# Optimization experiments

Hardware: AMD Instinct MI355X
Metric: run time of the kernel (lower is better)

Reference implementation:

```python
import jax, jax.numpy as jnp
import numpy as np

H = 16          # N_heads (Attention default)
DH = 32         # d per head (Attention default)
EPS = 1e-5      # torch LayerNorm eps
SCALE = float(1.0 / np.sqrt(DH))


def _ln(z, w, b):
    # LayerNorm over the last TWO dims (normalized_shape=(N_x, channel)), affine w/b of shape [2S, C]
    m = jnp.mean(z, axis=(-2, -1), keepdims=True)
    v = jnp.mean(jnp.square(z - m), axis=(-2, -1), keepdims=True)
    return (z - m) * jax.lax.rsqrt(v + EPS) * w + b


def _attention(a, p):
    # a: [2S, C]. Faithful to source: y = x.clone(), scores are NOT softmaxed (causal_mask=False).
    lx_w, lx_b, ly_w, ly_b, lf_w, lf_b, wq_w, wq_b, wk_w, wk_b, wv_w, wv_b, w1, b1, w2, b2, w3, b3 = p
    L = a.shape[0]
    xn = _ln(a, lx_w, lx_b)
    yn = _ln(a, ly_w, ly_b)
    q = (xn @ wq_w.T + wq_b).reshape(L, H, DH).transpose(1, 0, 2)  # [H, 2S, d]
    k = (yn @ wk_w.T + wk_b).reshape(L, H, DH).transpose(1, 0, 2)
    v = (yn @ wv_w.T + wv_b).reshape(L, H, DH).transpose(1, 0, 2)
    scores = jnp.einsum('hqd,hkd->hqk', q, k) * SCALE               # no softmax in source
    o = jnp.einsum('hqk,hkd->hqd', scores, v).transpose(1, 0, 2).reshape(L, H * DH)
    x1 = a + o @ w1.T + b1
    h = jax.nn.gelu(_ln(x1, lf_w, lf_b) @ w2.T + b2, approximate=False)
    return x1 + h @ w3.T + b3


def _forward(x, params):
    # x: [3, S, S, C]; params are stacked over the idx axis [S, ...] (one Attention per idx, shared across modes)
    S = x.shape[1]
    attn = jax.vmap(_attention, in_axes=(0, 0))
    for m1, m2 in [(0, 1), (2, 0), (1, 2)]:
        a = jnp.concatenate([x[m1], jnp.swapaxes(x[m2], 0, 1)], axis=1)  # [S, 2S, C]
        c = attn(a, params)                                              # [S, 2S, C]
        x = x.at[m1].set(c[:, :S, :])
        x = x.at[m2].set(c[:, S:, :])
    return x


def setup_inputs() -> dict:
    S, C, W = 16, 1024, 4
    D = H * DH   # 512
    L = 2 * S    # 32
    key = jax.random.key(0)
    ks = jax.random.split(key, 8)
    rn = lambda k, shp, s: jax.random.normal(k, shp, dtype=jnp.float32) * s
    return {
        'x': rn(ks[0], (3, S, S, C), 1.0),
        'lx_w': jnp.ones((S, L, C), jnp.float32), 'lx_b': jnp.zeros((S, L, C), jnp.float32),
        'ly_w': jnp.ones((S, L, C), jnp.float32), 'ly_b': jnp.zeros((S, L, C), jnp.float32),
        'lf_w': jnp.ones((S, L, C), jnp.float32), 'lf_b': jnp.zeros((S, L, C), jnp.float32),
        'wq_w': rn(ks[1], (S, D, C), 0.02), 'wq_b': jnp.zeros((S, D), jnp.float32),
        'wk_w': rn(ks[2], (S, D, C), 0.02), 'wk_b': jnp.zeros((S, D), jnp.float32),
        'wv_w': rn(ks[3], (S, D, C), 0.02), 'wv_b': jnp.zeros((S, D), jnp.float32),
        'w1': rn(ks[4], (S, C, D), 0.02), 'b1': jnp.zeros((S, C), jnp.float32),
        'w2': rn(ks[5], (S, W * C, C), 0.02), 'b2': jnp.zeros((S, W * C), jnp.float32),
        'w3': rn(ks[6], (S, C, W * C), 0.02), 'b3': jnp.zeros((S, C), jnp.float32),
    }


def reference(x, lx_w, lx_b, ly_w, ly_b, lf_w, lf_b, wq_w, wq_b, wk_w, wk_b, wv_w, wv_b, w1, b1, w2, b2, w3, b3):
    params = (lx_w, lx_b, ly_w, ly_b, lf_w, lf_b, wq_w, wq_b, wk_w, wk_b, wv_w, wv_b, w1, b1, w2, b2, w3, b3)
    return _forward(x, params)
```

## Files before the change

kernel.cpp:

```cpp
#include <hip/hip_runtime.h>


#define C1024 1024
#define D512  512
#define FF4096 4096
#define NELEM 32768.0f
#define EPSLN 1e-5f
#define QSCALE 0.17677669529663687f
#define LP 258

typedef __attribute__((ext_vector_type(8))) short bf16x8;
typedef __attribute__((ext_vector_type(4))) float f32x4;
typedef unsigned short u16;

__device__ inline u16 f2bf(float f) {
    unsigned u = __float_as_uint(f);
    u += 0x7fffu + ((u >> 16) & 1u);
    return (u16)(u >> 16);
}

__device__ inline bf16x8 cvt8(f32x4 a, f32x4 b) {
    bf16x8 r;
    r[0] = (short)f2bf(a[0]); r[1] = (short)f2bf(a[1]);
    r[2] = (short)f2bf(a[2]); r[3] = (short)f2bf(a[3]);
    r[4] = (short)f2bf(b[0]); r[5] = (short)f2bf(b[1]);
    r[6] = (short)f2bf(b[2]); r[7] = (short)f2bf(b[3]);
    return r;
}

struct Cvt4 {
    const float* s[4];
    u16* d[4];
    int N32[4], kzs[4], base[4];
};
__global__ void __launch_bounds__(256, 8) k_cvt6(Cvt4 a) {
    __shared__ float lds[16 * LP];
    int bid = blockIdx.x;
    int ts = 0;
#pragma unroll
    for (int j = 1; j < 4; ++j) if (bid >= a.base[j]) ts = j;
    int local = bid - a.base[ts];
    int kzs = a.kzs[ts], N32 = a.N32[ts];
    int kz = local % kzs;
    int b  = (local / kzs) & 1;
    int nt = (local / (kzs * 2)) % N32;
    int i  = local / (kzs * 2 * N32);
    int K = kzs * 256;
    int t = threadIdx.x;
    int row = t >> 4, c16 = t & 15;
    const float* Sp = a.s[ts] + ((size_t)((i * N32 + nt) * 32) + b * 16 + row) * K + kz * 256 + c16 * 4;
    float* Lrow = lds + row * LP + c16 * 4;
#pragma unroll
    for (int j = 0; j < 4; ++j) {
        f32x4 v = *(const f32x4*)(Sp + 64 * j);
        Lrow[64 * j]     = v[0];
        Lrow[64 * j + 1] = v[1];
        Lrow[64 * j + 2] = v[2];
        Lrow[64 * j + 3] = v[3];
    }
    __syncthreads();
    u16* Dp = a.d[ts] + (((size_t)(i * N32 + nt) * (kzs * 8) + kz * 8) * 1024) + b * 512;
#pragma unroll
    for (int p = 0; p < 2; ++p) {
        int u = p * 2048 + t * 8;
        int c   = u >> 9;
        int rem = u & 511;
        int kg = rem >> 7;
        int lr = (rem >> 3) & 15;
        const float* src = lds + lr * LP + c * 32 + kg * 8;
        f32x4 lo, hi;
        lo[0] = src[0]; lo[1] = src[1]; lo[2] = src[2]; lo[3] = src[3];
        hi[0] = src[4]; hi[1] = src[5]; hi[2] = src[6]; hi[3] = src[7];
        *(bf16x8*)(Dp + c * 1024 + rem) = cvt8(lo, hi);
    }
}

template<int EPI>
__global__ void __launch_bounds__(256, 4)
k_cvtgemm(const float* __restrict__ W32, u16* __restrict__ W16,
          const u16* __restrict__ act, int kzs, int N32,
          const float* __restrict__ bias,
          u16* __restrict__ hb,
          const float* __restrict__ x1, float* __restrict__ xout,
          int m1, int m2) {
    __shared__ float lds[16 * LP];
    __shared__ float Pl[4][32][16];
    int bx = blockIdx.x, i = blockIdx.y;
    int b = bx & 1, nt = bx >> 1;
    int K = kzs * 256;
    int t = threadIdx.x;
    int w = t >> 6, lane = t & 63;
    int lr = lane & 15, kg = lane >> 4;
    int row = t >> 4, c16 = t & 15;
    const float* Sp = W32 + ((size_t)(i * N32 + nt) * 32 + b * 16 + row) * K + c16 * 4;
    u16* Dbase = W16 + ((size_t)(i * N32 + nt) * (kzs * 8)) * 1024 + b * 512;
    const u16* A0 = act + ((size_t)(i * 32) + lr) * K + kg * 8;
    const u16* A1 = A0 + (size_t)16 * K;
    f32x4 acc0 = {0.f, 0.f, 0.f, 0.f}, acc1 = {0.f, 0.f, 0.f, 0.f};
    float* Lrow = lds + row * LP + c16 * 4;
    const float* src = lds + lr * LP + kg * 8;
    for (int kz = 0; kz < kzs; ++kz) {
        const float* Sk = Sp + kz * 256;
#pragma unroll
        for (int j = 0; j < 4; ++j) {
            f32x4 v = *(const f32x4*)(Sk + 64 * j);
            Lrow[64 * j]     = v[0];
            Lrow[64 * j + 1] = v[1];
            Lrow[64 * j + 2] = v[2];
            Lrow[64 * j + 3] = v[3];
        }
        __syncthreads();
        u16* Dp = Dbase + (size_t)(kz * 8) * 1024;
#pragma unroll
        for (int p = 0; p < 2; ++p) {
            int c = p * 4 + w;
            const float* s8 = src + c * 32;
            f32x4 lo, hi;
            lo[0] = s8[0]; lo[1] = s8[1]; lo[2] = s8[2]; lo[3] = s8[3];
            hi[0] = s8[4]; hi[1] = s8[5]; hi[2] = s8[6]; hi[3] = s8[7];
            bf16x8 r = cvt8(lo, hi);
            *(bf16x8*)(Dp + c * 1024 + lane * 8) = r;
            int kk = kz * 8 + c;
            bf16x8 aF0 = *(const bf16x8*)(A0 + kk * 32);
            bf16x8 aF1 = *(const bf16x8*)(A1 + kk * 32);
            acc0 = __builtin_amdgcn_mfma_f32_16x16x32_bf16(aF0, r, acc0, 0, 0, 0);
            acc1 = __builtin_amdgcn_mfma_f32_16x16x32_bf16(aF1, r, acc1, 0, 0, 0);
        }
        __syncthreads();
    }
#pragma unroll
    for (int rr = 0; rr < 4; ++rr) {
        Pl[w][kg * 4 + rr][lr]      = acc0[rr];
        Pl[w][16 + kg * 4 + rr][lr] = acc1[rr];
    }
    __syncthreads();
    int m = t >> 3, nl0 = (t & 7) * 2;
#pragma unroll
    for (int jj = 0; jj < 2; ++jj) {
        int nl = nl0 + jj;
        float v = Pl[0][m][nl] + Pl[1][m][nl] + Pl[2][m][nl] + Pl[3][m][nl];
        int n = nt * 32 + b * 16 + nl;
        if constexpr (EPI == 0) {
            float tt = v + bias[i * FF4096 + n];
            float g = 0.5f * tt * (1.f + erff(tt * 0.70710678118654752f));
            hb[((size_t)(i * 32) + m) * FF4096 + n] = f2bf(g);
        } else {
            int base = ((i * 32 + m) << 10) + n;
            float vv = v + bias[i * C1024 + n] + x1[base];
            int dst = (m < 16) ? (((m1 * 16 + i) * 16 + m) << 10)
                               : (((m2 * 16 + i) * 16 + (m - 16)) << 10);
            xout[dst + n] = vv;
        }
    }
}

__device__ inline void mmz(const u16* __restrict__ act, const u16* __restrict__ p,
                           int nkk, f32x4& acc0, f32x4& acc1) {
#pragma unroll 4
    for (int j = 0; j < nkk; ++j) {
        bf16x8 aF = *(const bf16x8*)(act + j * 32);
        bf16x8 b0 = *(const bf16x8*)(p + (size_t)j * 1024);
        bf16x8 b1 = *(const bf16x8*)(p + (size_t)j * 1024 + 512);
        acc0 = __builtin_amdgcn_mfma_f32_16x16x32_bf16(aF, b0, acc0, 0, 0, 0);
        acc1 = __builtin_amdgcn_mfma_f32_16x16x32_bf16(aF, b1, acc1, 0, 0, 0);
    }
}

__device__ inline void reduce256(float& s, float& q, int t, float* lds) {
    for (int off = 32; off; off >>= 1) {
        s += __shfl_down(s, off, 64);
        q += __shfl_down(q, off, 64);
    }
    int wv = t >> 6;
    if ((t & 63) == 0) { lds[wv * 2] = s; lds[wv * 2 + 1] = q; }
    __syncthreads();
    if (t == 0) {
        lds[8] = lds[0] + lds[2] + lds[4] + lds[6];
        lds[9] = lds[1] + lds[3] + lds[5] + lds[7];
    }
    __syncthreads();
    s = lds[8]; q = lds[9];
}

__global__ void k_ln1(const float* __restrict__ s1, const float* __restrict__ s2,
                      const float* __restrict__ gw, const float* __restrict__ gb,
                      const float* __restrict__ hw, const float* __restrict__ hb,
                      float* __restrict__ a_buf,
                      u16* __restrict__ xn, u16* __restrict__ yn) {
    __shared__ float lds[10];
    int i = blockIdx.x, cb = blockIdx.y, t = threadIdx.x;
    float s = 0.f, q = 0.f;
#pragma unroll 4
    for (int rr = 0; rr < 32; ++rr) {
        const float* src = (rr < 16)
            ? (s1 + ((i * 16 + rr) << 10))
            : (s2 + (((rr - 16) * 16 + i) << 10));
        f32x4 v = *(const f32x4*)(src + t * 4);
        s += v[0] + v[1] + v[2] + v[3];
        q += v[0]*v[0] + v[1]*v[1] + v[2]*v[2] + v[3]*v[3];
        if ((t >> 5) == cb)
            *(f32x4*)(a_buf + ((i * 32 + rr) << 10) + t * 4) = v;
    }
    reduce256(s, q, t, lds);
    float mean = s * (1.f / NELEM);
    float var = q * (1.f / NELEM) - mean * mean;
    float inv = rsqrtf(var + EPSLN);
    int c = cb * 128 + (t & 31) * 4;
    int r0 = (t >> 5) * 4;
#pragma unroll
    for (int rr = 0; rr < 4; ++rr) {
        int row = r0 + rr;
        const float* src = (row < 16)
            ? (s1 + ((i * 16 + row) << 10))
            : (s2 + (((row - 16) * 16 + i) << 10));
        f32x4 v = *(const f32x4*)(src + c);
        int base = ((i * 32 + row) << 10) + c;
        f32x4 gwv = *(const f32x4*)(gw + base);
        f32x4 gbv = *(const f32x4*)(gb + base);
        f32x4 hwv = *(const f32x4*)(hw + base);
        f32x4 hbv = *(const f32x4*)(hb + base);
        float z0 = (v[0]-mean)*inv, z1 = (v[1]-mean)*inv, z2 = (v[2]-mean)*inv, z3 = (v[3]-mean)*inv;
        uint2 a, b;
        a.x = (unsigned)f2bf(z0*gwv[0]+gbv[0]) | ((unsigned)f2bf(z1*gwv[1]+gbv[1]) << 16);
        a.y = (unsigned)f2bf(z2*gwv[2]+gbv[2]) | ((unsigned)f2bf(z3*gwv[3]+gbv[3]) << 16);
        b.x = (unsigned)f2bf(z0*hwv[0]+hbv[0]) | ((unsigned)f2bf(z1*hwv[1]+hbv[1]) << 16);
        b.y = (unsigned)f2bf(z2*hwv[2]+hbv[2]) | ((unsigned)f2bf(z3*hwv[3]+hbv[3]) << 16);
        *(uint2*)(xn + base) = a;
        *(uint2*)(yn + base) = b;
    }
}

__global__ void k_ln2(const float* __restrict__ x1,
                      const float* __restrict__ gw, const float* __restrict__ gb,
                      u16* __restrict__ out) {
    __shared__ float lds[10];
    int i = blockIdx.x, cb = blockIdx.y, t = threadIdx.x;
    float s = 0.f, q = 0.f;
#pragma unroll 4
    for (int rr = 0; rr < 32; ++rr) {
        f32x4 v = *(const f32x4*)(x1 + ((i * 32 + rr) << 10) + t * 4);
        s += v[0] + v[1] + v[2] + v[3];
        q += v[0]*v[0] + v[1]*v[1] + v[2]*v[2] + v[3]*v[3];
    }
    reduce256(s, q, t, lds);
    float mean = s * (1.f / NELEM);
    float var = q * (1.f / NELEM) - mean * mean;
    float inv = rsqrtf(var + EPSLN);
    int c = cb * 128 + (t & 31) * 4;
    int r0 = (t >> 5) * 4;
#pragma unroll
    for (int rr = 0; rr < 4; ++rr) {
        int base = ((i * 32 + r0 + rr) << 10) + c;
        f32x4 v  = *(const f32x4*)(x1 + base);
        f32x4 gwv = *(const f32x4*)(gw + base);
        f32x4 gbv = *(const f32x4*)(gb + base);
        float z0 = (v[0]-mean)*inv, z1 = (v[1]-mean)*inv, z2 = (v[2]-mean)*inv, z3 = (v[3]-mean)*inv;
        uint2 a;
        a.x = (unsigned)f2bf(z0*gwv[0]+gbv[0]) | ((unsigned)f2bf(z1*gwv[1]+gbv[1]) << 16);
        a.y = (unsigned)f2bf(z2*gwv[2]+gbv[2]) | ((unsigned)f2bf(z3*gwv[3]+gbv[3]) << 16);
        *(uint2*)(out + base) = a;
    }
}

__global__ void __launch_bounds__(512, 4)
k_gemm_qkv(const u16* __restrict__ xn, const u16* __restrict__ yn,
           const u16* __restrict__ wq, const float* __restrict__ wqb,
           const u16* __restrict__ wk, const float* __restrict__ wkb,
           const u16* __restrict__ wv, const float* __restrict__ wvb,
           u16* __restrict__ qo, u16* __restrict__ ko, u16* __restrict__ vT) {
    __shared__ float Pl[2][32][64];
    int bx = blockIdx.x, i = blockIdx.y;
    int w = threadIdx.x >> 6, lane = threadIdx.x & 63;
    int kh = w >> 2, mh = (w >> 1) & 1, wn = w & 1;
    int lr = lane & 15, kg = lane >> 4;
    int sel = bx >> 3;
    int ntl = (bx - sel * 8) * 2 + wn;
    const u16* act = (sel == 0 ? xn : yn) + (i * 32 + mh * 16 + lr) * C1024 + kh * 512 + kg * 8;
    const u16* Wm = (sel == 0 ? wq : (sel == 1 ? wk : wv));
    const u16* p = Wm + (((size_t)i * 16 + ntl) * 32 + kh * 16) * 1024 + lane * 8;
    f32x4 a0 = {0.f, 0.f, 0.f, 0.f}, a1 = {0.f, 0.f, 0.f, 0.f};
    mmz(act, p, 16, a0, a1);
    int m0 = mh * 16 + kg * 4;
#pragma unroll
    for (int r = 0; r < 4; ++r) {
        Pl[kh][m0 + r][wn * 32 + lr] = a0[r];
        Pl[kh][m0 + r][wn * 32 + 16 + lr] = a1[r];
    }
    __syncthreads();
    int t = threadIdx.x;
    int row = t >> 4, c0 = (t & 15) * 4;
    int nloc = bx * 64 - sel * 512 + c0;
    const float* bias = (sel == 0 ? wqb : (sel == 1 ? wkb : wvb)) + i * D512 + nloc;
    float v0 = Pl[0][row][c0]     + Pl[1][row][c0]     + bias[0];
    float v1 = Pl[0][row][c0 + 1] + Pl[1][row][c0 + 1] + bias[1];
    float v2 = Pl[0][row][c0 + 2] + Pl[1][row][c0 + 2] + bias[2];
    float v3 = Pl[0][row][c0 + 3] + Pl[1][row][c0 + 3] + bias[3];
    if (sel == 0) {
        uint2 a;
        a.x = (unsigned)f2bf(v0 * QSCALE) | ((unsigned)f2bf(v1 * QSCALE) << 16);
        a.y = (unsigned)f2bf(v2 * QSCALE) | ((unsigned)f2bf(v3 * QSCALE) << 16);
        *(uint2*)(qo + (i * 32 + row) * D512 + nloc) = a;
    } else if (sel == 1) {
        uint2 a;
        a.x = (unsigned)f2bf(v0) | ((unsigned)f2bf(v1) << 16);
        a.y = (unsigned)f2bf(v2) | ((unsigned)f2bf(v3) << 16);
        *(uint2*)(ko + (i * 32 + row) * D512 + nloc) = a;
    } else {
        int h = nloc >> 5, d = nloc & 31;
        u16* vb = vT + ((i * 16 + h) * 32 + d) * 32 + row;
        vb[0]  = f2bf(v0);
        vb[32] = f2bf(v1);
        vb[64] = f2bf(v2);
        vb[96] = f2bf(v3);
    }
}

__global__ void k_attn(const u16* __restrict__ q, const u16* __restrict__ k,
                       const u16* __restrict__ vT, u16* __restrict__ o) {
    __shared__ __align__(16) u16 Sm[4][32][32];
    int i = blockIdx.x;
    int w = threadIdx.x >> 6, lane = threadIdx.x & 63;
    int h = blockIdx.y * 4 + w;
    int lr = lane & 15, kg = lane >> 4;
    const u16* qb = q + i * 32 * D512 + h * 32 + kg * 8;
    const u16* kb = k + i * 32 * D512 + h * 32 + kg * 8;
    bf16x8 a0 = *(const bf16x8*)(qb + lr * D512);
    bf16x8 a1 = *(const bf16x8*)(qb + (16 + lr) * D512);
    bf16x8 b0 = *(const bf16x8*)(kb + lr * D512);
    bf16x8 b1 = *(const bf16x8*)(kb + (16 + lr) * D512);
    f32x4 z = {0.f, 0.f, 0.f, 0.f};
    f32x4 s00 = __builtin_amdgcn_mfma_f32_16x16x32_bf16(a0, b0, z, 0, 0, 0);
    f32x4 s01 = __builtin_amdgcn_mfma_f32_16x16x32_bf16(a0, b1, z, 0, 0, 0);
    f32x4 s10 = __builtin_amdgcn_mfma_f32_16x16x32_bf16(a1, b0, z, 0, 0, 0);
    f32x4 s11 = __builtin_amdgcn_mfma_f32_16x16x32_bf16(a1, b1, z, 0, 0, 0);
    int mr = kg * 4;
#pragma unroll
    for (int r = 0; r < 4; ++r) {
        Sm[w][mr + r][lr]           = f2bf(s00[r]);
        Sm[w][mr + r][16 + lr]      = f2bf(s01[r]);
        Sm[w][16 + mr + r][lr]      = f2bf(s10[r]);
        Sm[w][16 + mr + r][16 + lr] = f2bf(s11[r]);
    }
    __syncthreads();
    bf16x8 p0 = *(const bf16x8*)&Sm[w][lr][kg * 8];
    bf16x8 p1 = *(const bf16x8*)&Sm[w][16 + lr][kg * 8];
    const u16* vb = vT + (i * 16 + h) * 32 * 32 + kg * 8;
    bf16x8 v0 = *(const bf16x8*)(vb + lr * 32);
    bf16x8 v1 = *(const bf16x8*)(vb + (16 + lr) * 32);
    f32x4 o00 = __builtin_amdgcn_mfma_f32_16x16x32_bf16(p0, v0, z, 0, 0, 0);
    f32x4 o01 = __builtin_amdgcn_mfma_f32_16x16x32_bf16(p0, v1, z, 0, 0, 0);
    f32x4 o10 = __builtin_amdgcn_mfma_f32_16x16x32_bf16(p1, v0, z, 0, 0, 0);
    f32x4 o11 = __builtin_amdgcn_mfma_f32_16x16x32_bf16(p1, v1, z, 0, 0, 0);
#pragma unroll
    for (int r = 0; r < 4; ++r) {
        o[(i * 32 + mr + r) * D512 + h * 32 + lr]           = f2bf(o00[r]);
        o[(i * 32 + mr + r) * D512 + h * 32 + 16 + lr]      = f2bf(o01[r]);
        o[(i * 32 + 16 + mr + r) * D512 + h * 32 + lr]      = f2bf(o10[r]);
        o[(i * 32 + 16 + mr + r) * D512 + h * 32 + 16 + lr] = f2bf(o11[r]);
    }
}

__global__ void __launch_bounds__(512, 4)
k_gemm_w1(const u16* __restrict__ ob, const u16* __restrict__ W,
          const float* __restrict__ bias, const float* __restrict__ a_buf,
          float* __restrict__ x1) {
    __shared__ float Pl[2][32][64];
    int bx = blockIdx.x, i = blockIdx.y;
    int w = threadIdx.x >> 6, lane = threadIdx.x & 63;
    int kh = w >> 2, mh = (w >> 1) & 1, wn = w & 1;
    int lr = lane & 15, kg = lane >> 4;
    int nt = bx * 2 + wn;
    const u16* act = ob + (i * 32 + mh * 16 + lr) * D512 + kh * 256 + kg * 8;
    const u16* p = W + (((size_t)i * 32 + nt) * 16 + kh * 8) * 1024 + lane * 8;
    f32x4 a0 = {0.f, 0.f, 0.f, 0.f}, a1 = {0.f, 0.f, 0.f, 0.f};
    mmz(act, p, 8, a0, a1);
    int m0 = mh * 16 + kg * 4;
#pragma unroll
    for (int r = 0; r < 4; ++r) {
        Pl[kh][m0 + r][wn * 32 + lr] = a0[r];
        Pl[kh][m0 + r][wn * 32 + 16 + lr] = a1[r];
    }
    __syncthreads();
    int t = threadIdx.x;
    int row = t >> 4, c0 = (t & 15) * 4;
    int n = bx * 64 + c0;
    int base = ((i * 32 + row) << 10) + n;
    f32x4 bv = *(const f32x4*)(bias + i * C1024 + n);
    f32x4 av = *(const f32x4*)(a_buf + base);
    f32x4 r;
    r[0] = Pl[0][row][c0]     + Pl[1][row][c0]     + bv[0] + av[0];
    r[1] = Pl[0][row][c0 + 1] + Pl[1][row][c0 + 1] + bv[1] + av[1];
    r[2] = Pl[0][row][c0 + 2] + Pl[1][row][c0 + 2] + bv[2] + av[2];
    r[3] = Pl[0][row][c0 + 3] + Pl[1][row][c0 + 3] + bv[3] + av[3];
    *(f32x4*)(x1 + base) = r;
}

__global__ void __launch_bounds__(256, 4)
k_gemm_w2(const u16* __restrict__ lnf, const u16* __restrict__ W,
          const float* __restrict__ bias, u16* __restrict__ hb) {
    int bx = blockIdx.x, i = blockIdx.y;
    int w = threadIdx.x >> 6, lane = threadIdx.x & 63;
    int mh = w & 1, wn = w >> 1, lr = lane & 15, kg = lane >> 4;
    int nt = bx * 2 + wn;
    const u16* act = lnf + (i * 32 + mh * 16 + lr) * C1024 + kg * 8;
    const u16* p = W + (((size_t)i * 128 + nt) * 32) * 1024 + lane * 8;
    f32x4 a0 = {0.f, 0.f, 0.f, 0.f}, a1 = {0.f, 0.f, 0.f, 0.f};
    mmz(act, p, 32, a0, a1);
    int m0 = mh * 16 + kg * 4;
    int nb = bx * 64 + wn * 32;
    int n0 = nb + lr, n1 = nb + 16 + lr;
    float b0 = bias[i * FF4096 + n0], b1 = bias[i * FF4096 + n1];
#pragma unroll
    for (int r = 0; r < 4; ++r) {
        float t0 = a0[r] + b0;
        float t1 = a1[r] + b1;
        float g0 = 0.5f * t0 * (1.f + erff(t0 * 0.70710678118654752f));
        float g1 = 0.5f * t1 * (1.f + erff(t1 * 0.70710678118654752f));
        hb[(i * 32 + m0 + r) * FF4096 + n0] = f2bf(g0);
        hb[(i * 32 + m0 + r) * FF4096 + n1] = f2bf(g1);
    }
}

__global__ void __launch_bounds__(1024, 4)
k_gemm_w3(const u16* __restrict__ hb, const u16* __restrict__ W,
          const float* __restrict__ bias, const float* __restrict__ x1,
          float* __restrict__ xout, int m1, int m2) {
    __shared__ float Pl[4][32][64];
    int bx = blockIdx.x, i = blockIdx.y;
    int w = threadIdx.x >> 6, lane = threadIdx.x & 63;
    int kq = w >> 2, mh = (w >> 1) & 1, wn = w & 1;
    int lr = lane & 15, kg = lane >> 4;
    int nt = bx * 2 + wn;
    const u16* act = hb + (i * 32 + mh * 16 + lr) * FF4096 + kq * 1024 + kg * 8;
    const u16* p = W + (((size_t)i * 32 + nt) * 128 + kq * 32) * 1024 + lane * 8;
    f32x4 a0 = {0.f, 0.f, 0.f, 0.f}, a1 = {0.f, 0.f, 0.f, 0.f};
    mmz(act, p, 32, a0, a1);
    int m0 = mh * 16 + kg * 4;
#pragma unroll
    for (int r = 0; r < 4; ++r) {
        Pl[kq][m0 + r][wn * 32 + lr] = a0[r];
        Pl[kq][m0 + r][wn * 32 + 16 + lr] = a1[r];
    }
    __syncthreads();
    int t = threadIdx.x;
    int row = t >> 5, c0 = (t & 31) * 2;
    int n = bx * 64 + c0;
    int dst = (row < 16) ? (((m1 * 16 + i) * 16 + row) << 10)
                         : (((m2 * 16 + i) * 16 + (row - 16)) << 10);
    int base = ((i * 32 + row) << 10) + n;
#pragma unroll
    for (int j = 0; j < 2; ++j) {
        float v = Pl[0][row][c0 + j] + Pl[1][row][c0 + j]
                + Pl[2][row][c0 + j] + Pl[3][row][c0 + j]
                + bias[i * C1024 + n + j] + x1[base + j];
        xout[dst + n + j] = v;
    }
}

extern "C" void kernel_launch(void* const* d_in, const int* in_sizes, int n_in,
                              void* d_out, int out_size, void* d_ws, size_t ws_size,
                              hipStream_t stream) {
    const float* x_in = (const float*)d_in[0];
    const float* lx_w = (const float*)d_in[1];
    const float* lx_b = (const float*)d_in[2];
    const float* ly_w = (const float*)d_in[3];
    const float* ly_b = (const float*)d_in[4];
    const float* lf_w = (const float*)d_in[5];
    const float* lf_b = (const float*)d_in[6];
    const float* wq_w = (const float*)d_in[7];
    const float* wq_b = (const float*)d_in[8];
    const float* wk_w = (const float*)d_in[9];
    const float* wk_b = (const float*)d_in[10];
    const float* wv_w = (const float*)d_in[11];
    const float* wv_b = (const float*)d_in[12];
    const float* w1   = (const float*)d_in[13];
    const float* b1   = (const float*)d_in[14];
    const float* w2   = (const float*)d_in[15];
    const float* b2   = (const float*)d_in[16];
    const float* w3   = (const float*)d_in[17];
    const float* b3   = (const float*)d_in[18];

    float* xbuf = (float*)d_out;
    char* ws = (char*)d_ws;
    float* a_buf  = (float*)(ws);
    float* x1_buf = (float*)(ws + (2u << 20));
    u16*   xn     = (u16*)(ws + (4u << 20));
    u16*   yn     = (u16*)(ws + (5u << 20));
    u16*   lnf    = (u16*)(ws + (6u << 20));
    u16*   qb     = (u16*)(ws + (7u << 20));
    u16*   kb     = (u16*)(ws + 7 * (1u << 20) + (1u << 19));
    u16*   vT     = (u16*)(ws + (8u << 20));
    u16*   ob     = (u16*)(ws + 8 * (1u << 20) + (1u << 19));
    u16*   hbuf   = (u16*)(ws + (9u << 20));
    u16*   wq16   = (u16*)(ws + (16u  << 20));
    u16*   wk16   = (u16*)(ws + (32u  << 20));
    u16*   wv16   = (u16*)(ws + (48u  << 20));
    u16*   w1_16  = (u16*)(ws + (64u  << 20));
    u16*   w2_16  = (u16*)(ws + (80u  << 20));
    u16*   w3_16  = (u16*)(ws + (208u << 20));

    Cvt4 ca;
    ca.s[0] = wq_w; ca.d[0] = wq16;  ca.N32[0] = 16;  ca.kzs[0] = 4;  ca.base[0] = 0;
    ca.s[1] = wk_w; ca.d[1] = wk16;  ca.N32[1] = 16;  ca.kzs[1] = 4;  ca.base[1] = 2048;
    ca.s[2] = wv_w; ca.d[2] = wv16;  ca.N32[2] = 16;  ca.kzs[2] = 4;  ca.base[2] = 4096;
    ca.s[3] = w1;   ca.d[3] = w1_16; ca.N32[3] = 32;  ca.kzs[3] = 2;  ca.base[3] = 6144;
    k_cvt6<<<8192, 256, 0, stream>>>(ca);

    const size_t SLAB = (size_t)16 * 16 * 1024;
    const int modes[3][2] = {{0, 1}, {2, 0}, {1, 2}};
    for (int mi = 0; mi < 3; ++mi) {
        int m1 = modes[mi][0], m2 = modes[mi][1];
        const float* s1 = (mi == 2) ? (xbuf + m1 * SLAB) : (x_in + m1 * SLAB);
        const float* s2 = (mi == 0) ? (x_in + m2 * SLAB) : (xbuf + m2 * SLAB);
        k_ln1<<<dim3(16, 8), 256, 0, stream>>>(s1, s2, lx_w, lx_b, ly_w, ly_b, a_buf, xn, yn);
        k_gemm_qkv<<<dim3(24, 16), 512, 0, stream>>>(xn, yn, wq16, wq_b, wk16, wk_b, wv16, wv_b, qb, kb, vT);
        k_attn<<<dim3(16, 4), 256, 0, stream>>>(qb, kb, vT, ob);
        k_gemm_w1<<<dim3(16, 16), 512, 0, stream>>>(ob, w1_16, b1, a_buf, x1_buf);
        k_ln2<<<dim3(16, 8), 256, 0, stream>>>(x1_buf, lf_w, lf_b, lnf);
        if (mi == 0) {
            k_cvtgemm<0><<<dim3(256, 16), 256, 0, stream>>>(
                w2, w2_16, lnf, 4, 128, b2, hbuf, nullptr, nullptr, 0, 0);
            k_cvtgemm<1><<<dim3(64, 16), 256, 0, stream>>>(
                w3, w3_16, hbuf, 16, 32, b3, nullptr, x1_buf, xbuf, m1, m2);
        } else {
            k_gemm_w2<<<dim3(64, 16), 256, 0, stream>>>(lnf, w2_16, b2, hbuf);
            k_gemm_w3<<<dim3(16, 16), 1024, 0, stream>>>(hbuf, w3_16, b3, x1_buf, xbuf, m1, m2);
        }
    }
}
```

Baseline: 507.5 us.

## Fuse QKV and W1 weight conversion into first-pass GEMMs, prefetch weights

Removes the standalone fp32-to-bf16 conversion kernel for Wq/Wk/Wv/W1. Each weight is now converted inside the first mode's GEMM, which writes the bf16 copy while using it, the same way W2/W3 were already handled. This saves one full pass over those weights and one launch. The shared conversion-GEMM body also register-prefetches the next K-chunk of fp32 weights before the LDS conversion, so global loads overlap the MFMA work. In exchange, the first-mode QKV and W1 GEMMs use a slower narrow-tile path.

```diff
diff --git a/kernel.cpp b/kernel.cpp
--- a/kernel.cpp
+++ b/kernel.cpp
@@ -28,88 +28,33 @@
     return r;
 }
 
-struct Cvt4 {
-    const float* s[4];
-    u16* d[4];
-    int N32[4], kzs[4], base[4];
-};
-__global__ void __launch_bounds__(256, 8) k_cvt6(Cvt4 a) {
-    __shared__ float lds[16 * LP];
-    int bid = blockIdx.x;
-    int ts = 0;
-#pragma unroll
-    for (int j = 1; j < 4; ++j) if (bid >= a.base[j]) ts = j;
-    int local = bid - a.base[ts];
-    int kzs = a.kzs[ts], N32 = a.N32[ts];
-    int kz = local % kzs;
-    int b  = (local / kzs) & 1;
-    int nt = (local / (kzs * 2)) % N32;
-    int i  = local / (kzs * 2 * N32);
-    int K = kzs * 256;
-    int t = threadIdx.x;
+__device__ inline void cvtgemm_body(const float* __restrict__ Sp,
+                                    u16* __restrict__ Dbase,
+                                    const u16* __restrict__ A0,
+                                    const u16* __restrict__ A1,
+                                    int kzs, int t, int w, int lane,
+                                    float* lds, f32x4& acc0, f32x4& acc1) {
     int row = t >> 4, c16 = t & 15;
-    const float* Sp = a.s[ts] + ((size_t)((i * N32 + nt) * 32) + b * 16 + row) * K + kz * 256 + c16 * 4;
-    float* Lrow = lds + row * LP + c16 * 4;
-#pragma unroll
-    for (int j = 0; j < 4; ++j) {
-        f32x4 v = *(const f32x4*)(Sp + 64 * j);
-        Lrow[64 * j]     = v[0];
-        Lrow[64 * j + 1] = v[1];
-        Lrow[64 * j + 2] = v[2];
-        Lrow[64 * j + 3] = v[3];
-    }
-    __syncthreads();
-    u16* Dp = a.d[ts] + (((size_t)(i * N32 + nt) * (kzs * 8) + kz * 8) * 1024) + b * 512;
-#pragma unroll
-    for (int p = 0; p < 2; ++p) {
-        int u = p * 2048 + t * 8;
-        int c   = u >> 9;
-        int rem = u & 511;
-        int kg = rem >> 7;
-        int lr = (rem >> 3) & 15;
-        const float* src = lds + lr * LP + c * 32 + kg * 8;
-        f32x4 lo, hi;
-        lo[0] = src[0]; lo[1] = src[1]; lo[2] = src[2]; lo[3] = src[3];
-        hi[0] = src[4]; hi[1] = src[5]; hi[2] = src[6]; hi[3] = src[7];
-        *(bf16x8*)(Dp + c * 1024 + rem) = cvt8(lo, hi);
-    }
-}
-
-template<int EPI>
-__global__ void __launch_bounds__(256, 4)
-k_cvtgemm(const float* __restrict__ W32, u16* __restrict__ W16,
-          const u16* __restrict__ act, int kzs, int N32,
-          const float* __restrict__ bias,
-          u16* __restrict__ hb,
-          const float* __restrict__ x1, float* __restrict__ xout,
-          int m1, int m2) {
-    __shared__ float lds[16 * LP];
-    __shared__ float Pl[4][32][16];
-    int bx = blockIdx.x, i = blockIdx.y;
-    int b = bx & 1, nt = bx >> 1;
-    int K = kzs * 256;
-    int t = threadIdx.x;
-    int w = t >> 6, lane = t & 63;
-    int lr = lane & 15, kg = lane >> 4;
-    int row = t >> 4, c16 = t & 15;
-    const float* Sp = W32 + ((size_t)(i * N32 + nt) * 32 + b * 16 + row) * K + c16 * 4;
-    u16* Dbase = W16 + ((size_t)(i * N32 + nt) * (kzs * 8)) * 1024 + b * 512;
-    const u16* A0 = act + ((size_t)(i * 32) + lr) * K + kg * 8;
-    const u16* A1 = A0 + (size_t)16 * K;
-    f32x4 acc0 = {0.f, 0.f, 0.f, 0.f}, acc1 = {0.f, 0.f, 0.f, 0.f};
+    int lr = lane & 15, kg = lane >> 4;
     float* Lrow = lds + row * LP + c16 * 4;
     const float* src = lds + lr * LP + kg * 8;
+    f32x4 rv0 = *(const f32x4*)(Sp);
+    f32x4 rv1 = *(const f32x4*)(Sp + 64);
+    f32x4 rv2 = *(const f32x4*)(Sp + 128);
+    f32x4 rv3 = *(const f32x4*)(Sp + 192);
     for (int kz = 0; kz < kzs; ++kz) {
-        const float* Sk = Sp + kz * 256;
-#pragma unroll
-        for (int j = 0; j < 4; ++j) {
-            f32x4 v = *(const f32x4*)(Sk + 64 * j);
-            Lrow[64 * j]     = v[0];
-            Lrow[64 * j + 1] = v[1];
-            Lrow[64 * j + 2] = v[2];
-            Lrow[64 * j + 3] = v[3];
+        Lrow[0]   = rv0[0]; Lrow[1]   = rv0[1]; Lrow[2]   = rv0[2]; Lrow[3]   = rv0[3];
+        Lrow[64]  = rv1[0]; Lrow[65]  = rv1[1]; Lrow[66]  = rv1[2]; Lrow[67]  = rv1[3];
+        Lrow[128] = rv2[0]; Lrow[129] = rv2[1]; Lrow[130] = rv2[2]; Lrow[131] = rv2[3];
+        Lrow[192] = rv3[0]; Lrow[193] = rv3[1]; Lrow[194] = rv3[2]; Lrow[195] = rv3[3];
+        __syncthreads();
+        if (kz + 1 < kzs) {
+            const float* Sk = Sp + (kz + 1) * 256;
+            rv0 = *(const f32x4*)(Sk);
+            rv1 = *(const f32x4*)(Sk + 64);
+            rv2 = *(const f32x4*)(Sk + 128);
+            rv3 = *(const f32x4*)(Sk + 192);
         }
-        __syncthreads();
         u16* Dp = Dbase + (size_t)(kz * 8) * 1024;
 #pragma unroll
         for (int p = 0; p < 2; ++p) {
@@ -128,6 +73,31 @@
         }
         __syncthreads();
     }
+}
+
+template<int EPI>
+__global__ void __launch_bounds__(256, 4)
+k_cvtgemm(const float* __restrict__ W32, u16* __restrict__ W16,
+          const u16* __restrict__ act, int kzs, int N32,
+          const float* __restrict__ bias,
+          u16* __restrict__ hb,
+          const float* __restrict__ x1, float* __restrict__ xout,
+          const float* __restrict__ a_buf,
+          int m1, int m2) {
+    __shared__ float lds[16 * LP];
+    __shared__ float Pl[4][32][16];
+    int bx = blockIdx.x, i = blockIdx.y;
+    int b = bx & 1, nt = bx >> 1;
+    int K = kzs * 256;
+    int t = threadIdx.x;
+    int w = t >> 6, lane = t & 63;
+    int lr = lane & 15, kg = lane >> 4;
+    const float* Sp = W32 + ((size_t)(i * N32 + nt) * 32 + b * 16 + (t >> 4)) * K + (t & 15) * 4;
+    u16* Dbase = W16 + ((size_t)(i * N32 + nt) * (kzs * 8)) * 1024 + b * 512;
+    const u16* A0 = act + ((size_t)(i * 32) + lr) * K + kg * 8;
+    const u16* A1 = A0 + (size_t)16 * K;
+    f32x4 acc0 = {0.f, 0.f, 0.f, 0.f}, acc1 = {0.f, 0.f, 0.f, 0.f};
+    cvtgemm_body(Sp, Dbase, A0, A1, kzs, t, w, lane, lds, acc0, acc1);
 #pragma unroll
     for (int rr = 0; rr < 4; ++rr) {
         Pl[w][kg * 4 + rr][lr]      = acc0[rr];
@@ -144,12 +114,67 @@
             float tt = v + bias[i * FF4096 + n];
             float g = 0.5f * tt * (1.f + erff(tt * 0.70710678118654752f));
             hb[((size_t)(i * 32) + m) * FF4096 + n] = f2bf(g);
-        } else {
+        } else if constexpr (EPI == 1) {
             int base = ((i * 32 + m) << 10) + n;
             float vv = v + bias[i * C1024 + n] + x1[base];
             int dst = (m < 16) ? (((m1 * 16 + i) * 16 + m) << 10)
                                : (((m2 * 16 + i) * 16 + (m - 16)) << 10);
             xout[dst + n] = vv;
+        } else {
+            int base = ((i * 32 + m) << 10) + n;
+            xout[base] = v + bias[i * C1024 + n] + a_buf[base];
+        }
+    }
+}
+
+__global__ void __launch_bounds__(256, 4)
+k_cvtgemm_qkv(const float* __restrict__ wq32, const float* __restrict__ wk32,
+              const float* __restrict__ wv32,
+              u16* __restrict__ wq16, u16* __restrict__ wk16, u16* __restrict__ wv16,
+              const u16* __restrict__ xn, const u16* __restrict__ yn,
+              const float* __restrict__ wqb, const float* __restrict__ wkb,
+              const float* __restrict__ wvb,
+              u16* __restrict__ qo, u16* __restrict__ ko, u16* __restrict__ vT) {
+    __shared__ float lds[16 * LP];
+    __shared__ float Pl[4][32][16];
+    const int kzs = 4, N32 = 16, K = 1024;
+    int bx = blockIdx.x, i = blockIdx.y;
+    int sel = bx >> 5;
+    int bxl = bx & 31;
+    int b = bxl & 1, nt = bxl >> 1;
+    const float* W32 = (sel == 0 ? wq32 : (sel == 1 ? wk32 : wv32));
+    u16* W16 = (sel == 0 ? wq16 : (sel == 1 ? wk16 : wv16));
+    const u16* act = (sel == 0 ? xn : yn);
+    const float* bias = (sel == 0 ? wqb : (sel == 1 ? wkb : wvb));
+    int t = threadIdx.x;
+    int w = t >> 6, lane = t & 63;
+    int lr = lane & 15, kg = lane >> 4;
+    const float* Sp = W32 + ((size_t)(i * N32 + nt) * 32 + b * 16 + (t >> 4)) * K + (t & 15) * 4;
+    u16* Dbase = W16 + ((size_t)(i * N32 + nt) * (kzs * 8)) * 1024 + b * 512;
+    const u16* A0 = act + ((size_t)(i * 32) + lr) * K + kg * 8;
+    const u16* A1 = A0 + (size_t)16 * K;
+    f32x4 acc0 = {0.f, 0.f, 0.f, 0.f}, acc1 = {0.f, 0.f, 0.f, 0.f};
+    cvtgemm_body(Sp, Dbase, A0, A1, kzs, t, w, lane, lds, acc0, acc1);
+#pragma unroll
+    for (int rr = 0; rr < 4; ++rr) {
+        Pl[w][kg * 4 + rr][lr]      = acc0[rr];
+        Pl[w][16 + kg * 4 + rr][lr] = acc1[rr];
+    }
+    __syncthreads();
+    int m = t >> 3, nl0 = (t & 7) * 2;
+#pragma unroll
+    for (int jj = 0; jj < 2; ++jj) {
+        int nl = nl0 + jj;
+        float v = Pl[0][m][nl] + Pl[1][m][nl] + Pl[2][m][nl] + Pl[3][m][nl];
+        int n = nt * 32 + b * 16 + nl;
+        v += bias[i * D512 + n];
+        if (sel == 0) {
+            qo[(i * 32 + m) * D512 + n] = f2bf(v * QSCALE);
+        } else if (sel == 1) {
+            ko[(i * 32 + m) * D512 + n] = f2bf(v);
+        } else {
+            int h = n >> 5, d = n & 31;
+            vT[((i * 16 + h) * 32 + d) * 32 + m] = f2bf(v);
         }
     }
 }
@@ -499,13 +524,6 @@
     u16*   w2_16  = (u16*)(ws + (80u  << 20));
     u16*   w3_16  = (u16*)(ws + (208u << 20));
 
-    Cvt4 ca;
-    ca.s[0] = wq_w; ca.d[0] = wq16;  ca.N32[0] = 16;  ca.kzs[0] = 4;  ca.base[0] = 0;
-    ca.s[1] = wk_w; ca.d[1] = wk16;  ca.N32[1] = 16;  ca.kzs[1] = 4;  ca.base[1] = 2048;
-    ca.s[2] = wv_w; ca.d[2] = wv16;  ca.N32[2] = 16;  ca.kzs[2] = 4;  ca.base[2] = 4096;
-    ca.s[3] = w1;   ca.d[3] = w1_16; ca.N32[3] = 32;  ca.kzs[3] = 2;  ca.base[3] = 6144;
-    k_cvt6<<<8192, 256, 0, stream>>>(ca);
-
     const size_t SLAB = (size_t)16 * 16 * 1024;
     const int modes[3][2] = {{0, 1}, {2, 0}, {1, 2}};
     for (int mi = 0; mi < 3; ++mi) {
@@ -513,16 +531,23 @@
         const float* s1 = (mi == 2) ? (xbuf + m1 * SLAB) : (x_in + m1 * SLAB);
         const float* s2 = (mi == 0) ? (x_in + m2 * SLAB) : (xbuf + m2 * SLAB);
         k_ln1<<<dim3(16, 8), 256, 0, stream>>>(s1, s2, lx_w, lx_b, ly_w, ly_b, a_buf, xn, yn);
-        k_gemm_qkv<<<dim3(24, 16), 512, 0, stream>>>(xn, yn, wq16, wq_b, wk16, wk_b, wv16, wv_b, qb, kb, vT);
-        k_attn<<<dim3(16, 4), 256, 0, stream>>>(qb, kb, vT, ob);
-        k_gemm_w1<<<dim3(16, 16), 512, 0, stream>>>(ob, w1_16, b1, a_buf, x1_buf);
-        k_ln2<<<dim3(16, 8), 256, 0, stream>>>(x1_buf, lf_w, lf_b, lnf);
         if (mi == 0) {
+            k_cvtgemm_qkv<<<dim3(96, 16), 256, 0, stream>>>(
+                wq_w, wk_w, wv_w, wq16, wk16, wv16, xn, yn,
+                wq_b, wk_b, wv_b, qb, kb, vT);
+            k_attn<<<dim3(16, 4), 256, 0, stream>>>(qb, kb, vT, ob);
+            k_cvtgemm<2><<<dim3(64, 16), 256, 0, stream>>>(
+                w1, w1_16, ob, 2, 32, b1, nullptr, nullptr, x1_buf, a_buf, 0, 0);
+            k_ln2<<<dim3(16, 8), 256, 0, stream>>>(x1_buf, lf_w, lf_b, lnf);
             k_cvtgemm<0><<<dim3(256, 16), 256, 0, stream>>>(
-                w2, w2_16, lnf, 4, 128, b2, hbuf, nullptr, nullptr, 0, 0);
+                w2, w2_16, lnf, 4, 128, b2, hbuf, nullptr, nullptr, nullptr, 0, 0);
             k_cvtgemm<1><<<dim3(64, 16), 256, 0, stream>>>(
-                w3, w3_16, hbuf, 16, 32, b3, nullptr, x1_buf, xbuf, m1, m2);
+                w3, w3_16, hbuf, 16, 32, b3, nullptr, x1_buf, xbuf, nullptr, m1, m2);
         } else {
+            k_gemm_qkv<<<dim3(24, 16), 512, 0, stream>>>(xn, yn, wq16, wq_b, wk16, wk_b, wv16, wv_b, qb, kb, vT);
+            k_attn<<<dim3(16, 4), 256, 0, stream>>>(qb, kb, vT, ob);
+            k_gemm_w1<<<dim3(16, 16), 512, 0, stream>>>(ob, w1_16, b1, a_buf, x1_buf);
+            k_ln2<<<dim3(16, 8), 256, 0, stream>>>(x1_buf, lf_w, lf_b, lnf);
             k_gemm_w2<<<dim3(64, 16), 256, 0, stream>>>(lnf, w2_16, b2, hbuf);
             k_gemm_w3<<<dim3(16, 16), 1024, 0, stream>>>(hbuf, w3_16, b3, x1_buf, xbuf, m1, m2);
         }
```

After: 500.5 us. No clear change (-1.4%).
